# Performance work log

Measured on AMD Instinct MI355X. Metric: run time of the kernel, lower is better.

The kernel has to match this reference:

```python
import jax, jax.numpy as jnp
import numpy as np

D = 6            # tree depth: 63 nodes per tree, leaves-first level order
HL = 256         # lstm hidden dim
HM = 128         # mlp hid dim
OFFSETS = [0, 32, 48, 56, 60, 62]  # level l occupies [off, off+2**(D-1-l))


def _lin(k, fan_in, fan_out, scale=0.02):
    return jax.random.normal(k, (fan_in, fan_out), jnp.float32) * scale


def setup_inputs() -> dict:
    key = jax.random.key(0)
    ks = jax.random.split(key, 40)
    B, N = 1024, 63
    inp = {
        "op": jax.random.normal(ks[0], (B, N, 32), jnp.float32),
        "feat": jax.random.normal(ks[1], (B, N, 64), jnp.float32),
        "cond1": jax.random.normal(ks[2], (B, N, 256), jnp.float32),
        "cond2": jax.random.normal(ks[3], (B, N, 256), jnp.float32),
        "bitmap": jax.random.uniform(ks[4], (B, N, 1000), jnp.float32),
        "has_cond": jnp.ones((B, N), jnp.float32),
        # embeddings (stored [in, out], i.e. transposed torch Linear weight)
        "W_op": _lin(ks[5], 32, HM), "b_op": jnp.zeros((HM,), jnp.float32),
        "W_feat": _lin(ks[6], 64, HM), "b_feat": jnp.zeros((HM,), jnp.float32),
        "W_pred": _lin(ks[7], 256, HM), "b_pred": jnp.zeros((HM,), jnp.float32),
        "W_bm": _lin(ks[8], 1000, HM), "b_bm": jnp.zeros((HM,), jnp.float32),
        # node LSTM (torch layout: [4*HL, in])
        "W_ih": jax.random.normal(ks[9], (4 * HL, 5 * HM), jnp.float32) * 0.02,
        "b_ih": jnp.zeros((4 * HL,), jnp.float32),
        "W_hh": jax.random.normal(ks[10], (4 * HL, HL), jnp.float32) * 0.02,
        "b_hh": jnp.zeros((4 * HL,), jnp.float32),
        # descendant attention
        "W_wh": _lin(ks[11], HL, 64), "W_ext": _lin(ks[12], 5 * HM, 64),
        "W_a": _lin(ks[13], 64, 1),
        "W_ht": _lin(ks[14], HL, HL), "b_ht": jnp.zeros((HL,), jnp.float32),
        # output heads
        "W_c1": _lin(ks[15], HL, HM), "b_c1": jnp.zeros((HM,), jnp.float32),
        "W_c2": _lin(ks[16], HM, HM), "b_c2": jnp.zeros((HM,), jnp.float32),
        "W_c3": _lin(ks[17], HM, 1), "b_c3": jnp.zeros((1,), jnp.float32),
        "W_d1": _lin(ks[18], HL, HM), "b_d1": jnp.zeros((HM,), jnp.float32),
        "W_d2": _lin(ks[19], HM, HM), "b_d2": jnp.zeros((HM,), jnp.float32),
        "W_d3": _lin(ks[20], HM, 1), "b_d3": jnp.zeros((1,), jnp.float32),
    }
    return inp


def _tree_forward(op, feat, cond1, cond2, bitmap, has_cond,
                  W_op, b_op, W_feat, b_feat, W_pred, b_pred, W_bm, b_bm,
                  W_ih, b_ih, W_hh, b_hh, W_wh, W_ext, W_a, W_ht, b_ht):
    B = op.shape[0]
    # per-node 5*HM input vector (conditions are single Compare predicates)
    x = jnp.concatenate([
        op @ W_op + b_op,
        feat @ W_feat + b_feat,
        cond1 @ W_pred + b_pred,
        cond2 @ W_pred + b_pred,
        (bitmap @ W_bm + b_bm) * has_cond[..., None],
    ], axis=-1)                                        # [B, 63, 5*HM]

    hiddens, cells = [], []
    for l in range(D):
        n, off = 2 ** (D - 1 - l), OFFSETS[l]
        xl = x[:, off:off + n]                         # [B, n, 5*HM]
        if l == 0:  # leaves: no children, no descendants
            h0 = jnp.zeros((B, n, HL), x.dtype)
            c0 = h0
        else:
            # all descendant hiddens of each node, grouped per parent
            desc = jnp.concatenate(
                [hiddens[lp].reshape(B, n, 2 ** (l - lp), HL) for lp in range(l)],
                axis=2)                                # [B, n, M, HL]
            e = jnp.tanh(desc @ W_wh + (xl @ W_ext)[:, :, None, :])
            logits = (e @ W_a)[..., 0]                 # [B, n, M]
            w = jax.nn.softmax(logits, axis=-1)        # exp/sum(exp)
            pooled = jnp.einsum('bnm,bnmh->bnh', w, desc)
            h0 = jnp.tanh(pooled @ W_ht + b_ht)        # hidden_transformation
            c0 = 0.5 * cells[l - 1].reshape(B, n, 2, HL).sum(axis=2)  # avg child cells
        # single-step LSTM (torch gate order i, f, g, o)
        gates = xl @ W_ih.T + b_ih + h0 @ W_hh.T + b_hh
        i_, f_, g_, o_ = jnp.split(gates, 4, axis=-1)
        c = jax.nn.sigmoid(f_) * c0 + jax.nn.sigmoid(i_) * jnp.tanh(g_)
        h = jax.nn.sigmoid(o_) * jnp.tanh(c)
        hiddens.append(h)
        cells.append(c)
    return hiddens[-1][:, 0]                           # root hidden [B, HL]


def reference(op, feat, cond1, cond2, bitmap, has_cond,
              W_op, b_op, W_feat, b_feat, W_pred, b_pred, W_bm, b_bm,
              W_ih, b_ih, W_hh, b_hh, W_wh, W_ext, W_a, W_ht, b_ht,
              W_c1, b_c1, W_c2, b_c2, W_c3, b_c3,
              W_d1, b_d1, W_d2, b_d2, W_d3, b_d3):
    root = _tree_forward(op, feat, cond1, cond2, bitmap, has_cond,
                         W_op, b_op, W_feat, b_feat, W_pred, b_pred, W_bm, b_bm,
                         W_ih, b_ih, W_hh, b_hh, W_wh, W_ext, W_a, W_ht, b_ht)
    cost = jax.nn.sigmoid(jax.nn.relu(jax.nn.relu(root @ W_c1 + b_c1) @ W_c2 + b_c2) @ W_c3 + b_c3)
    card = jax.nn.sigmoid(jax.nn.relu(jax.nn.relu(root @ W_d1 + b_d1) @ W_d2 + b_d2) @ W_d3 + b_d3)
    return (cost, card)
```

## Files before the change

### kernel.cpp

```cpp
#include <hip/hip_runtime.h>
#include <math.h>

typedef unsigned short u16;
typedef __bf16 bf16x8 __attribute__((ext_vector_type(8)));
typedef float f32x4 __attribute__((ext_vector_type(4)));

static __device__ __forceinline__ float sigf(float x){ return 1.0f/(1.0f+expf(-x)); }
static __device__ __forceinline__ u16 f2bf(float f){
    unsigned u = __builtin_bit_cast(unsigned, f);
    unsigned r = u + 0x7FFFu + ((u >> 16) & 1u);
    return (u16)(r >> 16);
}
static __device__ __forceinline__ float b2f(u16 s){
    unsigned u = ((unsigned)s) << 16;
    return __builtin_bit_cast(float, u);
}

#define AS1 __attribute__((address_space(1)))
#define AS3 __attribute__((address_space(3)))
static __device__ __forceinline__ void gload16(const void* g, void* l){
    __builtin_amdgcn_global_load_lds((const AS1 void*)g, (AS3 void*)l, 16, 0, 0);
}

__global__ void prep_w(const float* __restrict__ W, u16* __restrict__ Wt,
                       int K, int N, int Kpad)
{
    int idx = blockIdx.x * 256 + threadIdx.x;
    if (idx >= N * Kpad) return;
    int n = idx / Kpad, k = idx - n * Kpad;
    Wt[idx] = (k < K) ? f2bf(W[(long)k * N + n]) : (u16)0;
}

__global__ void prep_g(const float* __restrict__ W_ih, const float* __restrict__ W_hh,
                       u16* __restrict__ Wt)
{
    int idx = blockIdx.x * 256 + threadIdx.x;
    int n = idx / 896, k = idx - n * 896;
    float v = (k < 640) ? W_ih[(long)n * 640 + k] : W_hh[(long)n * 256 + (k - 640)];
    Wt[idx] = f2bf(v);
}

template<bool AF32, int BN>
__launch_bounds__(256)
__global__ void gemm_bf16(const void* __restrict__ Aptr, const u16* __restrict__ Bt,
                          void* __restrict__ Cout, const float* __restrict__ bias,
                          const float* __restrict__ rowscale,
                          int Kreal, int Kpad, int lda, int ldc,
                          int permA, int act, int outBF16)
{
    constexpr int BM = 128, LDT = 40;
    constexpr int WM = (BN == 128) ? 2 : 4;
    constexpr int MI = BM / WM / 16;
    constexpr int NI = 4;
    __shared__ u16 As[BM * LDT];
    __shared__ u16 Bs[BN * LDT];

    const int tid = threadIdx.x;
    const int lane = tid & 63, wv = tid >> 6;
    const int r0 = blockIdx.x * BM, c0 = blockIdx.y * BN;
    const int wr = (wv % WM) * (BM / WM);
    const int wc = (wv / WM) * 64;
    const int l15 = lane & 15, q8 = (lane >> 4) * 8;

    f32x4 acc[MI][NI];
#pragma unroll
    for (int i = 0; i < MI; i++)
#pragma unroll
        for (int j = 0; j < NI; j++) acc[i][j] = (f32x4){0.f, 0.f, 0.f, 0.f};

    for (int kt = 0; kt < Kpad; kt += 32) {
        if (AF32) {
            const float* Ag = (const float*)Aptr;
#pragma unroll
            for (int p = 0; p < 4; p++) {
                int v = tid + p * 256;
                int row = v >> 3, kc = (v & 7) * 4;
                long ar = r0 + row;
                long arow = permA ? ((ar & 1023) * 63 + (ar >> 10)) : ar;
                int k = kt + kc;
                float4 val;
                if (k + 4 <= Kreal) {
                    val = *(const float4*)(Ag + arow * (long)lda + k);
                } else {
                    val.x = (k + 0 < Kreal) ? Ag[arow * (long)lda + k + 0] : 0.f;
                    val.y = (k + 1 < Kreal) ? Ag[arow * (long)lda + k + 1] : 0.f;
                    val.z = (k + 2 < Kreal) ? Ag[arow * (long)lda + k + 2] : 0.f;
                    val.w = (k + 3 < Kreal) ? Ag[arow * (long)lda + k + 3] : 0.f;
                }
                ushort4 o; o.x = f2bf(val.x); o.y = f2bf(val.y); o.z = f2bf(val.z); o.w = f2bf(val.w);
                *(ushort4*)&As[row * LDT + kc] = o;
            }
        } else {
            const u16* Ag = (const u16*)Aptr;
#pragma unroll
            for (int p = 0; p < 2; p++) {
                int v = tid + p * 256;
                int row = v >> 2, kc = (v & 3) * 8;
                long ar = r0 + row;
                *(int4*)&As[row * LDT + kc] = *(const int4*)(Ag + ar * (long)lda + kt + kc);
            }
        }
        constexpr int BCH = BN * 4 / 256;
#pragma unroll
        for (int p = 0; p < BCH; p++) {
            int v = tid + p * 256;
            int row = v >> 2, kc = (v & 3) * 8;
            *(int4*)&Bs[row * LDT + kc] = *(const int4*)(Bt + (long)(c0 + row) * Kpad + kt + kc);
        }
        __syncthreads();

        bf16x8 af[MI], bfr[NI];
#pragma unroll
        for (int mi = 0; mi < MI; mi++)
            af[mi] = *reinterpret_cast<const bf16x8*>(&As[(wr + mi * 16 + l15) * LDT + q8]);
#pragma unroll
        for (int ni = 0; ni < NI; ni++)
            bfr[ni] = *reinterpret_cast<const bf16x8*>(&Bs[(wc + ni * 16 + l15) * LDT + q8]);
#pragma unroll
        for (int mi = 0; mi < MI; mi++)
#pragma unroll
            for (int ni = 0; ni < NI; ni++)
                acc[mi][ni] = __builtin_amdgcn_mfma_f32_16x16x32_bf16(af[mi], bfr[ni], acc[mi][ni], 0, 0, 0);
        __syncthreads();
    }

#pragma unroll
    for (int mi = 0; mi < MI; mi++) {
#pragma unroll
        for (int ni = 0; ni < NI; ni++) {
#pragma unroll
            for (int r = 0; r < 4; r++) {
                int row = r0 + wr + mi * 16 + (lane >> 4) * 4 + r;
                int col = c0 + wc + ni * 16 + l15;
                float v = acc[mi][ni][r];
                if (bias) v += bias[col];
                if (act == 1) v = tanhf(v);
                if (rowscale) v *= rowscale[(row & 1023) * 63 + (row >> 10)];
                if (outBF16) ((u16*)Cout)[(long)row * ldc + col] = f2bf(v);
                else         ((float*)Cout)[(long)row * ldc + col] = v;
            }
        }
    }
}

__launch_bounds__(256)
__global__ void gemm_glds64(const u16* __restrict__ A, const u16* __restrict__ Bt,
                            float* __restrict__ Cout, int Kpad, int lda, int ldc)
{
    __shared__ u16 As[128 * 32];
    __shared__ u16 Bs[64 * 32];

    const int tid = threadIdx.x;
    const int lane = tid & 63, wv = tid >> 6;
    const long r0 = (long)blockIdx.x * 128;
    const int wr = wv * 32;
    const int l15 = lane & 15, q8 = (lane >> 4) * 8;
    const int crow = lane >> 2;
    const int ckc  = (lane & 3) * 8;

    f32x4 acc[2][4];
#pragma unroll
    for (int i = 0; i < 2; i++)
#pragma unroll
        for (int j = 0; j < 4; j++) acc[i][j] = (f32x4){0.f, 0.f, 0.f, 0.f};

    for (int kt = 0; kt < Kpad; kt += 32) {
#pragma unroll
        for (int i = 0; i < 2; i++) {
            int j = wv * 2 + i;
            int row = j * 16 + crow;
            gload16(A + (r0 + row) * lda + kt + ckc, &As[j * 512]);
        }
        {
            int row = wv * 16 + crow;
            gload16(Bt + (long)row * Kpad + kt + ckc, &Bs[wv * 512]);
        }
        __syncthreads();

        bf16x8 af[2], bfr[4];
#pragma unroll
        for (int mi = 0; mi < 2; mi++)
            af[mi] = *reinterpret_cast<const bf16x8*>(&As[(wr + mi * 16 + l15) * 32 + q8]);
#pragma unroll
        for (int ni = 0; ni < 4; ni++)
            bfr[ni] = *reinterpret_cast<const bf16x8*>(&Bs[(ni * 16 + l15) * 32 + q8]);
#pragma unroll
        for (int mi = 0; mi < 2; mi++)
#pragma unroll
            for (int ni = 0; ni < 4; ni++)
                acc[mi][ni] = __builtin_amdgcn_mfma_f32_16x16x32_bf16(af[mi], bfr[ni], acc[mi][ni], 0, 0, 0);
        __syncthreads();
    }

#pragma unroll
    for (int mi = 0; mi < 2; mi++)
#pragma unroll
        for (int ni = 0; ni < 4; ni++)
#pragma unroll
            for (int r = 0; r < 4; r++) {
                long row = r0 + wr + mi * 16 + (lane >> 4) * 4 + r;
                int col = ni * 16 + l15;
                Cout[row * ldc + col] = acc[mi][ni][r];
            }
}

__launch_bounds__(256)
__global__ void gates_glds(const u16* __restrict__ xl, const u16* __restrict__ h0,
                           const u16* __restrict__ Wt_g,
                           const float* __restrict__ b_ih, const float* __restrict__ b_hh,
                           const float* __restrict__ Cprev,
                           u16* __restrict__ Hbuf, float* __restrict__ Cbuf,
                           int offCur, int offPrev, int Ktot)
{
    __shared__ u16 smem[128 * 136];
    __shared__ float bias_s[4][32];
    u16* As = smem;
    u16* Bs = smem + 4096;
    u16* Gs = smem;

    const int tid = threadIdx.x;
    const int lane = tid & 63, wv = tid >> 6;
    const long r0 = (long)blockIdx.x * 128;
    const int by32 = blockIdx.y * 32;
    const int wr = (wv & 1) * 64, wc = (wv >> 1) * 64;
    const int l15 = lane & 15, q8 = (lane >> 4) * 8;
    const int crow = lane >> 2;
    const int ckc  = (lane & 3) * 8;

    if (tid < 128) {
        int g = tid >> 5, c = tid & 31;
        int gcol = g * 256 + by32 + c;
        bias_s[g][c] = b_ih[gcol] + b_hh[gcol];
    }

    f32x4 acc[4][4];
#pragma unroll
    for (int i = 0; i < 4; i++)
#pragma unroll
        for (int j = 0; j < 4; j++) acc[i][j] = (f32x4){0.f, 0.f, 0.f, 0.f};

    for (int kt = 0; kt < Ktot; kt += 32) {
#pragma unroll
        for (int i = 0; i < 2; i++) {
            int j = wv * 2 + i;
            int row = j * 16 + crow;
            long ar = r0 + row;
            int k = kt + ckc;
            const u16* src = (kt < 640) ? (xl + ar * 640 + k) : (h0 + ar * 256 + (k - 640));
            gload16(src, &As[j * 512]);
        }
#pragma unroll
        for (int i = 0; i < 2; i++) {
            int j = wv * 2 + i;
            int row = j * 16 + crow;
            long brow = (long)((row >> 5) * 256 + by32 + (row & 31));
            gload16(Wt_g + brow * 896 + kt + ckc, &Bs[j * 512]);
        }
        __syncthreads();

        bf16x8 af[4], bfr[4];
#pragma unroll
        for (int mi = 0; mi < 4; mi++)
            af[mi] = *reinterpret_cast<const bf16x8*>(&As[(wr + mi * 16 + l15) * 32 + q8]);
#pragma unroll
        for (int ni = 0; ni < 4; ni++)
            bfr[ni] = *reinterpret_cast<const bf16x8*>(&Bs[(wc + ni * 16 + l15) * 32 + q8]);
#pragma unroll
        for (int mi = 0; mi < 4; mi++)
#pragma unroll
            for (int ni = 0; ni < 4; ni++)
                acc[mi][ni] = __builtin_amdgcn_mfma_f32_16x16x32_bf16(af[mi], bfr[ni], acc[mi][ni], 0, 0, 0);
        __syncthreads();
    }

#pragma unroll
    for (int mi = 0; mi < 4; mi++)
#pragma unroll
        for (int ni = 0; ni < 4; ni++)
#pragma unroll
            for (int r = 0; r < 4; r++) {
                int lr = wr + mi * 16 + (lane >> 4) * 4 + r;
                int lc = wc + ni * 16 + l15;
                Gs[lr * 136 + lc] = f2bf(acc[mi][ni][r]);
            }
    __syncthreads();

#pragma unroll
    for (int i = 0; i < 16; i++) {
        int r = (tid >> 5) * 16 + i;
        int c = tid & 31;
        float iv = b2f(Gs[r * 136 + c])      + bias_s[0][c];
        float fv = b2f(Gs[r * 136 + 32 + c]) + bias_s[1][c];
        float gv = b2f(Gs[r * 136 + 64 + c]) + bias_s[2][c];
        float ov = b2f(Gs[r * 136 + 96 + c]) + bias_s[3][c];
        long rloc = r0 + r;
        int nd = (int)(rloc >> 10), bb = (int)(rloc & 1023);
        int gcol = by32 + c;
        float c0v = 0.f;
        if (Cprev) {
            long ch = ((long)(offPrev + nd * 2) * 1024 + bb) * 256 + gcol;
            c0v = 0.5f * (Cprev[ch] + Cprev[ch + 262144]);
        }
        float cv = sigf(fv) * c0v + sigf(iv) * tanhf(gv);
        float hv = sigf(ov) * tanhf(cv);
        long orow = ((long)offCur * 1024 + rloc) * 256 + gcol;
        Cbuf[orow] = cv;
        Hbuf[orow] = f2bf(hv);
    }
}

__launch_bounds__(256)
__global__ void attn_fused(const float* __restrict__ E, const float* __restrict__ xextall,
                           const float* __restrict__ W_a, const u16* __restrict__ Hbuf,
                           float* __restrict__ pooled, int level, int m, int off)
{
    const int blk = blockIdx.x;
    const int i = blk >> 10, bb = blk & 1023;
    const int tid = threadIdx.x;
    const int ln = tid & 63, wv = tid >> 6;
    __shared__ float xs[64];
    __shared__ float raw[64];
    __shared__ float wsm[64];

    if (tid < 64) xs[tid] = xextall[((long)(off + i) * 1024 + bb) * 64 + tid];
    __syncthreads();

    const float wa = W_a[ln];
    for (int dd = wv; dd < m; dd += 4) {
        int lp = 0, cum = 0;
        for (;;) { int sz = 1 << (level - lp); if (dd < cum + sz) break; cum += sz; lp++; }
        int sz = 1 << (level - lp);
        int q = dd - cum;
        long row = (long)((64 - (64 >> lp)) + i * sz + q) * 1024 + bb;
        float v = tanhf(E[row * 64 + ln] + xs[ln]) * wa;
#pragma unroll
        for (int s = 32; s; s >>= 1) v += __shfl_xor(v, s);
        if (ln == 0) raw[dd] = v;
    }
    __syncthreads();

    if (tid < 64) {
        float v = (tid < m) ? raw[tid] : -1e30f;
        float mx = v;
#pragma unroll
        for (int s = 32; s; s >>= 1) mx = fmaxf(mx, __shfl_xor(mx, s));
        float e = (tid < m) ? expf(v - mx) : 0.f;
        float sum = e;
#pragma unroll
        for (int s = 32; s; s >>= 1) sum += __shfl_xor(sum, s);
        wsm[tid] = e / sum;
    }
    __syncthreads();

    float accv = 0.f;
    int cum = 0;
    for (int lp = 0; lp < level; lp++) {
        int sz = 1 << (level - lp);
        int base = 64 - (64 >> lp);
        for (int q = 0; q < sz; q++) {
            long row = (long)(base + i * sz + q) * 1024 + bb;
            accv = fmaf(wsm[cum + q], b2f(Hbuf[row * 256 + tid]), accv);
        }
        cum += sz;
    }
    pooled[(long)blk * 256 + tid] = accv;
}

__launch_bounds__(256)
__global__ void heads_kernel(const u16* __restrict__ Hbuf,
                             const float* __restrict__ W_c1, const float* __restrict__ b_c1,
                             const float* __restrict__ W_c2, const float* __restrict__ b_c2,
                             const float* __restrict__ W_c3, const float* __restrict__ b_c3,
                             const float* __restrict__ W_d1, const float* __restrict__ b_d1,
                             const float* __restrict__ W_d2, const float* __restrict__ b_d2,
                             const float* __restrict__ W_d3, const float* __restrict__ b_d3,
                             float* __restrict__ out)
{
    const int bb = blockIdx.x, tid = threadIdx.x;
    __shared__ float root[256];
    __shared__ float t1[128];
    __shared__ float t2[128];
    __shared__ float red[256];
    root[tid] = b2f(Hbuf[((long)62 * 1024 + bb) * 256 + tid]);
    __syncthreads();
    for (int head = 0; head < 2; head++) {
        const float* w1  = head ? W_d1 : W_c1;
        const float* bi1 = head ? b_d1 : b_c1;
        const float* w2  = head ? W_d2 : W_c2;
        const float* bi2 = head ? b_d2 : b_c2;
        const float* w3  = head ? W_d3 : W_c3;
        const float* bi3 = head ? b_d3 : b_c3;
        if (tid < 128) {
            float s = bi1[tid];
            for (int k = 0; k < 256; k++) s = fmaf(root[k], w1[k * 128 + tid], s);
            t1[tid] = fmaxf(s, 0.f);
        }
        __syncthreads();
        if (tid < 128) {
            float s = bi2[tid];
            for (int k = 0; k < 128; k++) s = fmaf(t1[k], w2[k * 128 + tid], s);
            t2[tid] = fmaxf(s, 0.f);
        }
        __syncthreads();
        red[tid] = (tid < 128) ? t2[tid] * w3[tid] : 0.f;
        __syncthreads();
        for (int s = 128; s; s >>= 1) { if (tid < s) red[tid] += red[tid + s]; __syncthreads(); }
        if (tid == 0) out[head * 1024 + bb] = sigf(red[0] + bi3[0]);
        __syncthreads();
    }
}

extern "C" void kernel_launch(void* const* d_in, const int* in_sizes, int n_in,
                              void* d_out, int out_size, void* d_ws, size_t ws_size,
                              hipStream_t stream)
{
    (void)in_sizes; (void)n_in; (void)out_size;
    const float* op       = (const float*)d_in[0];
    const float* feat     = (const float*)d_in[1];
    const float* cond1    = (const float*)d_in[2];
    const float* cond2    = (const float*)d_in[3];
    const float* bitmap   = (const float*)d_in[4];
    const float* has_cond = (const float*)d_in[5];
    const float* W_op     = (const float*)d_in[6];
    const float* b_op     = (const float*)d_in[7];
    const float* W_feat   = (const float*)d_in[8];
    const float* b_feat   = (const float*)d_in[9];
    const float* W_pred   = (const float*)d_in[10];
    const float* b_pred   = (const float*)d_in[11];
    const float* W_bm     = (const float*)d_in[12];
    const float* b_bm     = (const float*)d_in[13];
    const float* W_ih     = (const float*)d_in[14];
    const float* b_ih     = (const float*)d_in[15];
    const float* W_hh     = (const float*)d_in[16];
    const float* b_hh     = (const float*)d_in[17];
    const float* W_wh     = (const float*)d_in[18];
    const float* W_ext    = (const float*)d_in[19];
    const float* W_a      = (const float*)d_in[20];
    const float* W_ht     = (const float*)d_in[21];
    const float* b_ht     = (const float*)d_in[22];
    const float* W_c1     = (const float*)d_in[23];
    const float* b_c1     = (const float*)d_in[24];
    const float* W_c2     = (const float*)d_in[25];
    const float* b_c2     = (const float*)d_in[26];
    const float* W_c3     = (const float*)d_in[27];
    const float* b_c3     = (const float*)d_in[28];
    const float* W_d1     = (const float*)d_in[29];
    const float* b_d1     = (const float*)d_in[30];
    const float* W_d2     = (const float*)d_in[31];
    const float* b_d2     = (const float*)d_in[32];
    const float* W_d3     = (const float*)d_in[33];
    const float* b_d3     = (const float*)d_in[34];
    float* out = (float*)d_out;

    char* p = (char*)d_ws;
    auto alloc = [&](size_t bytes) -> char* {
        char* r = p; p += (bytes + 255) & ~(size_t)255; return r;
    };
    u16*   xall    = (u16*)  alloc((size_t)64512 * 640 * 2);
    float* xextall = (float*)alloc((size_t)64512 * 64 * 4);
    u16*   Hbuf    = (u16*)  alloc((size_t)64512 * 256 * 2);
    float* Cbuf    = (float*)alloc((size_t)64512 * 256 * 4);
    float* Ebuf    = (float*)alloc((size_t)62 * 1024 * 64 * 4);
    float* pooled  = (float*)alloc((size_t)16384 * 256 * 4);
    u16*   h0      = (u16*)  alloc((size_t)16384 * 256 * 2);
    u16*   Wt_op   = (u16*)  alloc((size_t)128 * 32 * 2);
    u16*   Wt_feat = (u16*)  alloc((size_t)128 * 64 * 2);
    u16*   Wt_pred = (u16*)  alloc((size_t)128 * 256 * 2);
    u16*   Wt_bm   = (u16*)  alloc((size_t)128 * 1024 * 2);
    u16*   Wt_g    = (u16*)  alloc((size_t)1024 * 896 * 2);
    u16*   Wt_wh   = (u16*)  alloc((size_t)64 * 256 * 2);
    u16*   Wt_ext  = (u16*)  alloc((size_t)64 * 640 * 2);
    u16*   Wt_ht   = (u16*)  alloc((size_t)256 * 256 * 2);
    if (ws_size < (size_t)(p - (char*)d_ws)) return;

    prep_w<<<16,  256, 0, stream>>>(W_op,   Wt_op,   32,   128, 32);
    prep_w<<<32,  256, 0, stream>>>(W_feat, Wt_feat, 64,   128, 64);
    prep_w<<<128, 256, 0, stream>>>(W_pred, Wt_pred, 256,  128, 256);
    prep_w<<<512, 256, 0, stream>>>(W_bm,   Wt_bm,   1000, 128, 1024);
    prep_w<<<64,  256, 0, stream>>>(W_wh,   Wt_wh,   256,  64,  256);
    prep_w<<<160, 256, 0, stream>>>(W_ext,  Wt_ext,  640,  64,  640);
    prep_w<<<256, 256, 0, stream>>>(W_ht,   Wt_ht,   256,  256, 256);
    prep_g<<<3584,256, 0, stream>>>(W_ih, W_hh, Wt_g);

    gemm_bf16<true,128><<<dim3(504,1), 256, 0, stream>>>(op,     Wt_op,   (void*)(xall + 0),   b_op,   nullptr,  32,   32,   32,   640, 1, 0, 1);
    gemm_bf16<true,128><<<dim3(504,1), 256, 0, stream>>>(feat,   Wt_feat, (void*)(xall + 128), b_feat, nullptr,  64,   64,   64,   640, 1, 0, 1);
    gemm_bf16<true,128><<<dim3(504,1), 256, 0, stream>>>(cond1,  Wt_pred, (void*)(xall + 256), b_pred, nullptr,  256,  256,  256,  640, 1, 0, 1);
    gemm_bf16<true,128><<<dim3(504,1), 256, 0, stream>>>(cond2,  Wt_pred, (void*)(xall + 384), b_pred, nullptr,  256,  256,  256,  640, 1, 0, 1);
    gemm_bf16<true,128><<<dim3(504,1), 256, 0, stream>>>(bitmap, Wt_bm,   (void*)(xall + 512), b_bm,   has_cond, 1000, 1024, 1000, 640, 1, 0, 1);
    gemm_glds64<<<504, 256, 0, stream>>>(xall, Wt_ext, xextall, 640, 640, 64);

    for (int l = 0; l < 6; l++) {
        const int n   = 32 >> l;
        const int off = 64 - (64 >> l);
        const int M   = n * 1024;
        const int m   = (2 << l) - 2;

        if (l > 0) {
            attn_fused<<<M, 256, 0, stream>>>(Ebuf, xextall, W_a, Hbuf, pooled, l, m, off);
            gemm_bf16<true,128><<<dim3(M/128, 2), 256, 0, stream>>>(pooled, Wt_ht, (void*)h0, b_ht, nullptr, 256, 256, 256, 256, 0, 1, 1);
        }

        const int Ktot    = l ? 896 : 640;
        const int offPrev = l ? (64 - (64 >> (l - 1))) : 0;
        gates_glds<<<dim3(M/128, 8), 256, 0, stream>>>(xall + (size_t)off * 1024 * 640, h0, Wt_g,
                                                       b_ih, b_hh, l ? Cbuf : nullptr,
                                                       Hbuf, Cbuf, off, offPrev, Ktot);

        if (l < 5) {
            gemm_glds64<<<M/128, 256, 0, stream>>>(Hbuf + (size_t)off * 1024 * 256, Wt_wh,
                                                   Ebuf + (size_t)off * 1024 * 64, 256, 256, 64);
        }
    }

    heads_kernel<<<1024, 256, 0, stream>>>(Hbuf, W_c1, b_c1, W_c2, b_c2, W_c3, b_c3,
                                           W_d1, b_d1, W_d2, b_d2, W_d3, b_d3, out);
}
```

Baseline: 1.316 ms.

## Interleave LSTM gate weights and compute gate epilogue in registers

Weight prep now reorders the concatenated LSTM weight rows so the four gates of each hidden cell sit next to each other. The gates kernel moves to 512 threads with a 128x256 output tile and a swizzled 1D grid, so the activation tile is loaded half as many times. Its epilogue uses lane shuffles to collect each cell's i/f/g/o values in registers, which removes the LDS staging and the bf16 rounding of the gate values. Separately, the attention pooled output is stored in bf16, and the W_ht projection now runs on the generalised gemm_glds64 kernel with bias, tanh and bf16 output. The cost is higher register and LDS pressure per block and more shuffle instructions in the epilogue.

```diff
diff --git a/kernel.cpp b/kernel.cpp
--- a/kernel.cpp
+++ b/kernel.cpp
@@ -35,8 +35,9 @@
                        u16* __restrict__ Wt)
 {
     int idx = blockIdx.x * 256 + threadIdx.x;
-    int n = idx / 896, k = idx - n * 896;
-    float v = (k < 640) ? W_ih[(long)n * 640 + k] : W_hh[(long)n * 256 + (k - 640)];
+    int np = idx / 896, k = idx - np * 896;
+    int n_old = (np & 3) * 256 + (np >> 2);
+    float v = (k < 640) ? W_ih[(long)n_old * 640 + k] : W_hh[(long)n_old * 256 + (k - 640)];
     Wt[idx] = f2bf(v);
 }
 
@@ -145,14 +146,23 @@
 
 __launch_bounds__(256)
 __global__ void gemm_glds64(const u16* __restrict__ A, const u16* __restrict__ Bt,
-                            float* __restrict__ Cout, int Kpad, int lda, int ldc)
+                            void* __restrict__ Cout, const float* __restrict__ bias,
+                            int Kpad, int lda, int ldc, int act, int outBF16, int swz)
 {
     __shared__ u16 As[128 * 32];
     __shared__ u16 Bs[64 * 32];
 
     const int tid = threadIdx.x;
     const int lane = tid & 63, wv = tid >> 6;
-    const long r0 = (long)blockIdx.x * 128;
+    int bx = blockIdx.x, by = blockIdx.y;
+    if (swz) {
+        int wg = by * gridDim.x + bx;
+        int t = wg >> 3;
+        bx = (wg & 7) + 8 * (t >> 2);
+        by = t & 3;
+    }
+    const long r0 = (long)bx * 128;
+    const int c0 = by * 64;
     const int wr = wv * 32;
     const int l15 = lane & 15, q8 = (lane >> 4) * 8;
     const int crow = lane >> 2;
@@ -173,7 +183,7 @@
         }
         {
             int row = wv * 16 + crow;
-            gload16(Bt + (long)row * Kpad + kt + ckc, &Bs[wv * 512]);
+            gload16(Bt + (long)(c0 + row) * Kpad + kt + ckc, &Bs[wv * 512]);
         }
         __syncthreads();
 
@@ -199,38 +209,46 @@
 #pragma unroll
             for (int r = 0; r < 4; r++) {
                 long row = r0 + wr + mi * 16 + (lane >> 4) * 4 + r;
-                int col = ni * 16 + l15;
-                Cout[row * ldc + col] = acc[mi][ni][r];
+                int col = c0 + ni * 16 + l15;
+                float v = acc[mi][ni][r];
+                if (bias) v += bias[col];
+                if (act == 1) v = tanhf(v);
+                if (outBF16) ((u16*)Cout)[row * ldc + col] = f2bf(v);
+                else         ((float*)Cout)[row * ldc + col] = v;
             }
 }
 
-__launch_bounds__(256)
+__launch_bounds__(512, 4)
 __global__ void gates_glds(const u16* __restrict__ xl, const u16* __restrict__ h0,
-                           const u16* __restrict__ Wt_g,
+                           const u16* __restrict__ Wt_gi,
                            const float* __restrict__ b_ih, const float* __restrict__ b_hh,
                            const float* __restrict__ Cprev,
                            u16* __restrict__ Hbuf, float* __restrict__ Cbuf,
                            int offCur, int offPrev, int Ktot)
 {
-    __shared__ u16 smem[128 * 136];
-    __shared__ float bias_s[4][32];
-    u16* As = smem;
-    u16* Bs = smem + 4096;
-    u16* Gs = smem;
+    __shared__ u16 As[128 * 32];
+    __shared__ u16 Bs[256 * 32];
+    __shared__ float bias_s[256];
 
     const int tid = threadIdx.x;
     const int lane = tid & 63, wv = tid >> 6;
-    const long r0 = (long)blockIdx.x * 128;
-    const int by32 = blockIdx.y * 32;
+    {
+    }
+    int wg = blockIdx.x;
+    int t = wg >> 3;
+    const int bx = (wg & 7) + 8 * (t >> 2);
+    const int by = t & 3;
+    const long r0 = (long)bx * 128;
+    const int c0cell = by * 64;
     const int wr = (wv & 1) * 64, wc = (wv >> 1) * 64;
     const int l15 = lane & 15, q8 = (lane >> 4) * 8;
     const int crow = lane >> 2;
     const int ckc  = (lane & 3) * 8;
 
-    if (tid < 128) {
-        int g = tid >> 5, c = tid & 31;
-        int gcol = g * 256 + by32 + c;
-        bias_s[g][c] = b_ih[gcol] + b_hh[gcol];
+    if (tid < 256) {
+        int j = tid;
+        int gcol_old = (j & 3) * 256 + c0cell + (j >> 2);
+        bias_s[j] = b_ih[gcol_old] + b_hh[gcol_old];
     }
 
     f32x4 acc[4][4];
@@ -240,21 +258,18 @@
         for (int j = 0; j < 4; j++) acc[i][j] = (f32x4){0.f, 0.f, 0.f, 0.f};
 
     for (int kt = 0; kt < Ktot; kt += 32) {
-#pragma unroll
-        for (int i = 0; i < 2; i++) {
-            int j = wv * 2 + i;
-            int row = j * 16 + crow;
+        {
+            int row = wv * 16 + crow;
             long ar = r0 + row;
             int k = kt + ckc;
             const u16* src = (kt < 640) ? (xl + ar * 640 + k) : (h0 + ar * 256 + (k - 640));
-            gload16(src, &As[j * 512]);
+            gload16(src, &As[wv * 512]);
         }
 #pragma unroll
         for (int i = 0; i < 2; i++) {
-            int j = wv * 2 + i;
-            int row = j * 16 + crow;
-            long brow = (long)((row >> 5) * 256 + by32 + (row & 31));
-            gload16(Wt_g + brow * 896 + kt + ckc, &Bs[j * 512]);
+            int j2 = wv * 2 + i;
+            int row = j2 * 16 + crow;
+            gload16(Wt_gi + (long)(by * 256 + row) * 896 + kt + ckc, &Bs[j2 * 512]);
         }
         __syncthreads();
 
@@ -273,46 +288,54 @@
         __syncthreads();
     }
 
-#pragma unroll
-    for (int mi = 0; mi < 4; mi++)
-#pragma unroll
-        for (int ni = 0; ni < 4; ni++)
-#pragma unroll
-            for (int r = 0; r < 4; r++) {
-                int lr = wr + mi * 16 + (lane >> 4) * 4 + r;
-                int lc = wc + ni * 16 + l15;
-                Gs[lr * 136 + lc] = f2bf(acc[mi][ni][r]);
+    const int pq = lane & 1, pq2 = lane & 2;
+#pragma unroll
+    for (int mi = 0; mi < 4; mi++) {
+#pragma unroll
+        for (int ni = 0; ni < 4; ni++) {
+            float v0 = acc[mi][ni][0], v1 = acc[mi][ni][1];
+            float v2 = acc[mi][ni][2], v3 = acc[mi][ni][3];
+            float t0 = __shfl_xor(v1, 1);
+            float t1 = __shfl_xor(v0, 1);
+            float t2 = __shfl_xor(v3, 1);
+            float t3 = __shfl_xor(v2, 1);
+            float a0 = pq  ? t0 : v0;
+            float a1 = pq  ? v1 : t1;
+            float a2 = pq  ? t2 : v2;
+            float a3 = pq  ? v3 : t3;
+            float u0 = __shfl_xor(a2, 2);
+            float u1 = __shfl_xor(a3, 2);
+            float u2 = __shfl_xor(a0, 2);
+            float u3 = __shfl_xor(a1, 2);
+            float w0 = pq2 ? u0 : a0;
+            float w1 = pq2 ? u1 : a1;
+            float w2 = pq2 ? a2 : u2;
+            float w3 = pq2 ? a3 : u3;
+            int row = wr + mi * 16 + (lane >> 4) * 4 + (l15 & 3);
+            int cl  = ((wc + ni * 16) >> 2) + (l15 >> 2);
+            float4 bi = *(const float4*)&bias_s[cl * 4];
+            float iv = w0 + bi.x, fv = w1 + bi.y, gv = w2 + bi.z, ov = w3 + bi.w;
+            long rloc = r0 + row;
+            int nd = (int)(rloc >> 10), bb = (int)(rloc & 1023);
+            int gcol = c0cell + cl;
+            float c0v = 0.f;
+            if (Cprev) {
+                long ch = ((long)(offPrev + nd * 2) * 1024 + bb) * 256 + gcol;
+                c0v = 0.5f * (Cprev[ch] + Cprev[ch + 262144]);
             }
-    __syncthreads();
-
-#pragma unroll
-    for (int i = 0; i < 16; i++) {
-        int r = (tid >> 5) * 16 + i;
-        int c = tid & 31;
-        float iv = b2f(Gs[r * 136 + c])      + bias_s[0][c];
-        float fv = b2f(Gs[r * 136 + 32 + c]) + bias_s[1][c];
-        float gv = b2f(Gs[r * 136 + 64 + c]) + bias_s[2][c];
-        float ov = b2f(Gs[r * 136 + 96 + c]) + bias_s[3][c];
-        long rloc = r0 + r;
-        int nd = (int)(rloc >> 10), bb = (int)(rloc & 1023);
-        int gcol = by32 + c;
-        float c0v = 0.f;
-        if (Cprev) {
-            long ch = ((long)(offPrev + nd * 2) * 1024 + bb) * 256 + gcol;
-            c0v = 0.5f * (Cprev[ch] + Cprev[ch + 262144]);
-        }
-        float cv = sigf(fv) * c0v + sigf(iv) * tanhf(gv);
-        float hv = sigf(ov) * tanhf(cv);
-        long orow = ((long)offCur * 1024 + rloc) * 256 + gcol;
-        Cbuf[orow] = cv;
-        Hbuf[orow] = f2bf(hv);
+            float cv = sigf(fv) * c0v + sigf(iv) * tanhf(gv);
+            float hv = sigf(ov) * tanhf(cv);
+            long orow = ((long)offCur * 1024 + rloc) * 256 + gcol;
+            Cbuf[orow] = cv;
+            Hbuf[orow] = f2bf(hv);
+        }
     }
 }
 
 __launch_bounds__(256)
 __global__ void attn_fused(const float* __restrict__ E, const float* __restrict__ xextall,
                            const float* __restrict__ W_a, const u16* __restrict__ Hbuf,
-                           float* __restrict__ pooled, int level, int m, int off)
+                           u16* __restrict__ pooled, int level, int m, int off)
 {
     const int blk = blockIdx.x;
     const int i = blk >> 10, bb = blk & 1023;
@@ -363,7 +386,7 @@
         }
         cum += sz;
     }
-    pooled[(long)blk * 256 + tid] = accv;
+    pooled[(long)blk * 256 + tid] = f2bf(accv);
 }
 
 __launch_bounds__(256)
@@ -461,7 +484,7 @@
     u16*   Hbuf    = (u16*)  alloc((size_t)64512 * 256 * 2);
     float* Cbuf    = (float*)alloc((size_t)64512 * 256 * 4);
     float* Ebuf    = (float*)alloc((size_t)62 * 1024 * 64 * 4);
-    float* pooled  = (float*)alloc((size_t)16384 * 256 * 4);
+    u16*   pooled  = (u16*)  alloc((size_t)16384 * 256 * 2);
     u16*   h0      = (u16*)  alloc((size_t)16384 * 256 * 2);
     u16*   Wt_op   = (u16*)  alloc((size_t)128 * 32 * 2);
     u16*   Wt_feat = (u16*)  alloc((size_t)128 * 64 * 2);
@@ -487,7 +510,7 @@
     gemm_bf16<true,128><<<dim3(504,1), 256, 0, stream>>>(cond1,  Wt_pred, (void*)(xall + 256), b_pred, nullptr,  256,  256,  256,  640, 1, 0, 1);
     gemm_bf16<true,128><<<dim3(504,1), 256, 0, stream>>>(cond2,  Wt_pred, (void*)(xall + 384), b_pred, nullptr,  256,  256,  256,  640, 1, 0, 1);
     gemm_bf16<true,128><<<dim3(504,1), 256, 0, stream>>>(bitmap, Wt_bm,   (void*)(xall + 512), b_bm,   has_cond, 1000, 1024, 1000, 640, 1, 0, 1);
-    gemm_glds64<<<504, 256, 0, stream>>>(xall, Wt_ext, xextall, 640, 640, 64);
+    gemm_glds64<<<dim3(504,1), 256, 0, stream>>>(xall, Wt_ext, (void*)xextall, nullptr, 640, 640, 64, 0, 0, 0);
 
     for (int l = 0; l < 6; l++) {
         const int n   = 32 >> l;
@@ -497,18 +520,19 @@
 
         if (l > 0) {
             attn_fused<<<M, 256, 0, stream>>>(Ebuf, xextall, W_a, Hbuf, pooled, l, m, off);
-            gemm_bf16<true,128><<<dim3(M/128, 2), 256, 0, stream>>>(pooled, Wt_ht, (void*)h0, b_ht, nullptr, 256, 256, 256, 256, 0, 1, 1);
+            gemm_glds64<<<dim3(M/128, 4), 256, 0, stream>>>(pooled, Wt_ht, (void*)h0, b_ht, 256, 256, 256, 1, 1, 1);
         }
 
         const int Ktot    = l ? 896 : 640;
         const int offPrev = l ? (64 - (64 >> (l - 1))) : 0;
-        gates_glds<<<dim3(M/128, 8), 256, 0, stream>>>(xall + (size_t)off * 1024 * 640, h0, Wt_g,
-                                                       b_ih, b_hh, l ? Cbuf : nullptr,
-                                                       Hbuf, Cbuf, off, offPrev, Ktot);
+        gates_glds<<<(M/128) * 4, 512, 0, stream>>>(xall + (size_t)off * 1024 * 640, h0, Wt_g,
+                                                    b_ih, b_hh, l ? Cbuf : nullptr,
+                                                    Hbuf, Cbuf, off, offPrev, Ktot);
 
         if (l < 5) {
-            gemm_glds64<<<M/128, 256, 0, stream>>>(Hbuf + (size_t)off * 1024 * 256, Wt_wh,
-                                                   Ebuf + (size_t)off * 1024 * 64, 256, 256, 64);
+            gemm_glds64<<<dim3(M/128, 1), 256, 0, stream>>>(Hbuf + (size_t)off * 1024 * 256, Wt_wh,
+                                                            (void*)(Ebuf + (size_t)off * 1024 * 64),
+                                                            nullptr, 256, 256, 64, 0, 0, 0);
         }
     }
 
```

After: 1.203 ms. 8.6% less time.
